# Kernel tuning notes

Measured on AMD Instinct MI355X. Metric: run time of the kernel, lower is better.

## Reference

```python
import jax, jax.numpy as jnp
import numpy as np

TAU = 0.2  # temperature from __init__
EPS = 1e-12  # F.normalize eps


def setup_inputs() -> dict:
    key = jax.random.key(0)
    k1, k2, k3 = jax.random.split(key, 3)
    N, D = 131072, 1024
    return {
        "query": jax.random.normal(k1, (D,), dtype=jnp.float32),
        "K": jax.random.normal(k2, (N, D), dtype=jnp.float32),
        "V": jax.random.normal(k3, (N, D), dtype=jnp.float32),
        "topk": 32,
    }


def reference(query, K, V, topk):
    # q = F.normalize(query, dim=-1)
    q = query / jnp.maximum(jnp.linalg.norm(query, axis=-1, keepdims=True), EPS)
    # logits: [N] cosine-sim / tau (K rows are assumed pre-normalized by write())
    logits = (K @ q) / TAU
    # top-k branch (N > topk)
    vals, idxs = jax.lax.top_k(logits, topk)          # [topk], [topk]
    attn = jax.nn.softmax(vals, axis=-1)              # [topk]
    out = attn @ V[idxs]                              # [D]
    full_attn = jnp.zeros_like(logits).at[idxs].set(attn)  # [N]
    return out, full_attn
```

## Files before the change

### kernel.cpp

```cpp
#include <hip/hip_runtime.h>
#include <float.h>
#include <math.h>

#define DIM    1024
#define NROWS  131072
#define TOPK   32
#define TAU    0.2f
#define CHUNK  512
#define NCHUNK (NROWS / CHUNK)
#define NCAND  (NCHUNK * TOPK)

#define LOG_BLOCKS 2048
#define ROWS_PER_WAVE 16
#define NITER 8

typedef float floatx4 __attribute__((ext_vector_type(4)));

__device__ __forceinline__ floatx4 ld_nt(const float* p) {
    return __builtin_nontemporal_load(reinterpret_cast<const floatx4*>(p));
}

__global__ __launch_bounds__(256) void logits_kernel(const float* __restrict__ Km,
                                                     const float* __restrict__ q,
                                                     float* __restrict__ logits,
                                                     float* __restrict__ full_attn) {
    const int t    = threadIdx.x;
    const int lane = t & 63;
    const int wave = t >> 6;
    const int sub  = lane & 31;
    const int rsel = lane >> 5;

    floatx4 qv[8];
    #pragma unroll
    for (int p = 0; p < 8; ++p)
        qv[p] = *reinterpret_cast<const floatx4*>(q + p * 128 + sub * 4);

    const int gwave = blockIdx.x * 4 + wave;
    const int rbase = gwave * ROWS_PER_WAVE;
    const float* kptr = Km + (size_t)(rbase + rsel) * DIM + sub * 4;

    floatx4 buf[2][8];
    #pragma unroll
    for (int p = 0; p < 8; ++p)
        buf[0][p] = ld_nt(kptr + p * 128);

    #pragma unroll
    for (int r = 0; r < NITER; ++r) {
        const float* knext = kptr + 2 * DIM;
        if (r < NITER - 1) {
            #pragma unroll
            for (int p = 0; p < 8; ++p)
                buf[(r + 1) & 1][p] = ld_nt(knext + p * 128);
        }
        float a0 = 0.f, a1 = 0.f, a2 = 0.f, a3 = 0.f;
        #pragma unroll
        for (int p = 0; p < 8; ++p) {
            floatx4 kv = buf[r & 1][p];
            floatx4 qq = qv[p];
            a0 = fmaf(kv.x, qq.x, a0);
            a1 = fmaf(kv.y, qq.y, a1);
            a2 = fmaf(kv.z, qq.z, a2);
            a3 = fmaf(kv.w, qq.w, a3);
        }
        float acc = (a0 + a1) + (a2 + a3);
        #pragma unroll
        for (int off = 1; off < 32; off <<= 1) acc += __shfl_xor(acc, off, 64);
        if (sub == 0) {
            const int row = rbase + 2 * r + rsel;
            logits[row]    = acc;
            full_attn[row] = 0.f;
        }
        kptr = knext;
    }
}

__global__ __launch_bounds__(64) void topk_local_kernel(const float* __restrict__ logits,
                                                        float* __restrict__ cand_val,
                                                        int* __restrict__ cand_idx) {
    const int lane = threadIdx.x;
    const int base = blockIdx.x * CHUNK;

    float v[8]; int gi[8];
    floatx4 a = *reinterpret_cast<const floatx4*>(logits + base + lane * 4);
    floatx4 b = *reinterpret_cast<const floatx4*>(logits + base + 256 + lane * 4);
    v[0] = a.x; v[1] = a.y; v[2] = a.z; v[3] = a.w;
    v[4] = b.x; v[5] = b.y; v[6] = b.z; v[7] = b.w;
    #pragma unroll
    for (int j = 0; j < 4; ++j) gi[j] = base + lane * 4 + j;
    #pragma unroll
    for (int j = 0; j < 4; ++j) gi[4 + j] = base + 256 + lane * 4 + j;

    for (int r = 0; r < TOPK; ++r) {
        float m = v[0]; int mi = gi[0];
        #pragma unroll
        for (int j = 1; j < 8; ++j)
            if (v[j] > m || (v[j] == m && gi[j] < mi)) { m = v[j]; mi = gi[j]; }
        #pragma unroll
        for (int off = 32; off > 0; off >>= 1) {
            float ov = __shfl_xor(m, off, 64);
            int   oi = __shfl_xor(mi, off, 64);
            if (ov > m || (ov == m && oi < mi)) { m = ov; mi = oi; }
        }
        #pragma unroll
        for (int j = 0; j < 8; ++j)
            if (gi[j] == mi) v[j] = -FLT_MAX;
        if (lane == 0) {
            cand_val[blockIdx.x * TOPK + r] = m;
            cand_idx[blockIdx.x * TOPK + r] = mi;
        }
    }
}

__global__ __launch_bounds__(256) void final_kernel(const float* __restrict__ cand_val,
                                                    const int* __restrict__ cand_idx,
                                                    const float* __restrict__ q,
                                                    const float* __restrict__ Vm,
                                                    float* __restrict__ out,
                                                    float* __restrict__ full_attn) {
    const int t = threadIdx.x;
    const int lane = t & 63, wave = t >> 6;
    __shared__ float wred_v[4];
    __shared__ int   wred_i[4];
    __shared__ float tval[TOPK];
    __shared__ int   tidx[TOPK];
    __shared__ float attn_s[TOPK];
    __shared__ float red4[4];
    __shared__ float scale_s;

    float ss = 0.f;
    for (int i = t; i < DIM; i += 256) { float vq = q[i]; ss = fmaf(vq, vq, ss); }
    #pragma unroll
    for (int off = 32; off > 0; off >>= 1) ss += __shfl_xor(ss, off, 64);
    if (lane == 0) red4[wave] = ss;
    __syncthreads();
    if (t == 0) {
        float s = red4[0] + red4[1] + red4[2] + red4[3];
        scale_s = 1.0f / (fmaxf(sqrtf(s), 1e-12f) * TAU);
    }

    float v[32]; int gi[32];
    #pragma unroll
    for (int k = 0; k < 32; ++k) {
        int c = t + 256 * k;
        v[k]  = cand_val[c];
        gi[k] = cand_idx[c];
    }
    float m = v[0]; int mi = gi[0];
    #pragma unroll
    for (int k = 1; k < 32; ++k)
        if (v[k] > m || (v[k] == m && gi[k] < mi)) { m = v[k]; mi = gi[k]; }

    __syncthreads();

    for (int r = 0; r < TOPK; ++r) {
        float wm = m; int wmi = mi;
        #pragma unroll
        for (int off = 32; off > 0; off >>= 1) {
            float ov = __shfl_xor(wm, off, 64);
            int   oi = __shfl_xor(wmi, off, 64);
            if (ov > wm || (ov == wm && oi < wmi)) { wm = ov; wmi = oi; }
        }
        if (lane == 0) { wred_v[wave] = wm; wred_i[wave] = wmi; }
        __syncthreads();
        float gm = wred_v[0]; int gmi = wred_i[0];
        #pragma unroll
        for (int w = 1; w < 4; ++w) {
            float ov = wred_v[w]; int oi = wred_i[w];
            if (ov > gm || (ov == gm && oi < gmi)) { gm = ov; gmi = oi; }
        }
        if (t == 0) { tval[r] = gm; tidx[r] = gmi; }
        if (mi == gmi) {
            #pragma unroll
            for (int k = 0; k < 32; ++k)
                if (gi[k] == gmi) v[k] = -FLT_MAX;
            m = v[0]; mi = gi[0];
            #pragma unroll
            for (int k = 1; k < 32; ++k)
                if (v[k] > m || (v[k] == m && gi[k] < mi)) { m = v[k]; mi = gi[k]; }
        }
        __syncthreads();
    }

    const float scale = scale_s;
    float sum = 0.f;
    #pragma unroll
    for (int j = 0; j < TOPK; ++j) sum += expf((tval[j] - tval[0]) * scale);
    if (t < TOPK) attn_s[t] = expf((tval[t] - tval[0]) * scale) / sum;
    __syncthreads();

    if (t < TOPK) full_attn[tidx[t]] = attn_s[t];

    for (int d = t; d < DIM; d += 256) {
        float acc = 0.f;
        #pragma unroll
        for (int j = 0; j < TOPK; ++j)
            acc = fmaf(attn_s[j], Vm[(size_t)tidx[j] * DIM + d], acc);
        out[d] = acc;
    }
}

extern "C" void kernel_launch(void* const* d_in, const int* in_sizes, int n_in,
                              void* d_out, int out_size, void* d_ws, size_t ws_size,
                              hipStream_t stream) {
    const float* q  = (const float*)d_in[0];
    const float* Km = (const float*)d_in[1];
    const float* Vm = (const float*)d_in[2];

    float* out       = (float*)d_out;
    float* full_attn = out + DIM;

    float* logits   = (float*)d_ws;
    float* cand_val = logits + NROWS;
    int*   cand_idx = (int*)(cand_val + NCAND);

    logits_kernel<<<LOG_BLOCKS, 256, 0, stream>>>(Km, q, logits, full_attn);
    topk_local_kernel<<<NCHUNK, 64, 0, stream>>>(logits, cand_val, cand_idx);
    final_kernel<<<1, 256, 0, stream>>>(cand_val, cand_idx, q, Vm, out, full_attn);
}
```

Measured before the change: 187.8 us.

## Split logits GEMV into per-lane partial sums plus separate reduction kernel

```diff
diff --git a/kernel.cpp b/kernel.cpp
--- a/kernel.cpp
+++ b/kernel.cpp
@@ -10,9 +10,8 @@
 #define NCHUNK (NROWS / CHUNK)
 #define NCAND  (NCHUNK * TOPK)
 
-#define LOG_BLOCKS 2048
-#define ROWS_PER_WAVE 16
-#define NITER 8
+#define NWAVES 8192
+#define WSTEPS 16
 
 typedef float floatx4 __attribute__((ext_vector_type(4)));
 
@@ -20,57 +19,70 @@
     return __builtin_nontemporal_load(reinterpret_cast<const floatx4*>(p));
 }
 
-__global__ __launch_bounds__(256) void logits_kernel(const float* __restrict__ Km,
-                                                     const float* __restrict__ q,
-                                                     float* __restrict__ logits,
-                                                     float* __restrict__ full_attn) {
+__global__ __launch_bounds__(256) void logitsA_kernel(const float* __restrict__ Km,
+                                                      const float* __restrict__ q,
+                                                      float* __restrict__ partial) {
     const int t    = threadIdx.x;
     const int lane = t & 63;
     const int wave = t >> 6;
-    const int sub  = lane & 31;
-    const int rsel = lane >> 5;
-
-    floatx4 qv[8];
-    #pragma unroll
-    for (int p = 0; p < 8; ++p)
-        qv[p] = *reinterpret_cast<const floatx4*>(q + p * 128 + sub * 4);
-
     const int gwave = blockIdx.x * 4 + wave;
-    const int rbase = gwave * ROWS_PER_WAVE;
-    const float* kptr = Km + (size_t)(rbase + rsel) * DIM + sub * 4;
-
-    floatx4 buf[2][8];
-    #pragma unroll
-    for (int p = 0; p < 8; ++p)
-        buf[0][p] = ld_nt(kptr + p * 128);
-
-    #pragma unroll
-    for (int r = 0; r < NITER; ++r) {
-        const float* knext = kptr + 2 * DIM;
-        if (r < NITER - 1) {
+
+    floatx4 qv[4];
+    #pragma unroll
+    for (int j = 0; j < 4; ++j)
+        qv[j] = *reinterpret_cast<const floatx4*>(q + j * 256 + lane * 4);
+
+    const float* base = Km + (size_t)gwave * DIM + lane * 4;
+    floatx4 b[2][4];
+    #pragma unroll
+    for (int j = 0; j < 4; ++j) b[0][j] = ld_nt(base + j * 256);
+
+    float part[WSTEPS];
+    #pragma unroll
+    for (int w = 0; w < WSTEPS; ++w) {
+        const float* nbase = base + (size_t)NWAVES * DIM;
+        if (w < WSTEPS - 1) {
             #pragma unroll
-            for (int p = 0; p < 8; ++p)
-                buf[(r + 1) & 1][p] = ld_nt(knext + p * 128);
+            for (int j = 0; j < 4; ++j) b[(w + 1) & 1][j] = ld_nt(nbase + j * 256);
         }
         float a0 = 0.f, a1 = 0.f, a2 = 0.f, a3 = 0.f;
         #pragma unroll
-        for (int p = 0; p < 8; ++p) {
-            floatx4 kv = buf[r & 1][p];
-            floatx4 qq = qv[p];
+        for (int j = 0; j < 4; ++j) {
+            floatx4 kv = b[w & 1][j];
+            floatx4 qq = qv[j];
             a0 = fmaf(kv.x, qq.x, a0);
             a1 = fmaf(kv.y, qq.y, a1);
             a2 = fmaf(kv.z, qq.z, a2);
             a3 = fmaf(kv.w, qq.w, a3);
         }
-        float acc = (a0 + a1) + (a2 + a3);
-        #pragma unroll
-        for (int off = 1; off < 32; off <<= 1) acc += __shfl_xor(acc, off, 64);
-        if (sub == 0) {
-            const int row = rbase + 2 * r + rsel;
-            logits[row]    = acc;
+        part[w] = (a0 + a1) + (a2 + a3);
+        base = nbase;
+    }
+    #pragma unroll
+    for (int w = 0; w < WSTEPS; ++w)
+        partial[(size_t)(gwave + NWAVES * w) * 64 + lane] = part[w];
+}
+
+__global__ __launch_bounds__(256) void reduceB_kernel(const float* __restrict__ partial,
+                                                      float* __restrict__ logits,
+                                                      float* __restrict__ full_attn) {
+    const int t    = threadIdx.x;
+    const int lane = t & 63;
+    const int wave = t >> 6;
+    const int gw   = blockIdx.x * 4 + wave;
+    const int rowbase = gw * 32;
+
+    #pragma unroll
+    for (int it = 0; it < 8; ++it) {
+        const int row = rowbase + it * 4 + (lane >> 4);
+        floatx4 v = *reinterpret_cast<const floatx4*>(partial + (size_t)row * 64 + (lane & 15) * 4);
+        float s = (v.x + v.y) + (v.z + v.w);
+        #pragma unroll
+        for (int off = 1; off < 16; off <<= 1) s += __shfl_xor(s, off, 64);
+        if ((lane & 15) == 0) {
+            logits[row]    = s;
             full_attn[row] = 0.f;
         }
-        kptr = knext;
     }
 }
 
@@ -212,8 +224,10 @@
     float* logits   = (float*)d_ws;
     float* cand_val = logits + NROWS;
     int*   cand_idx = (int*)(cand_val + NCAND);
-
-    logits_kernel<<<LOG_BLOCKS, 256, 0, stream>>>(Km, q, logits, full_attn);
+    float* partial  = (float*)(cand_idx + NCAND);
+
+    logitsA_kernel<<<NWAVES / 4, 256, 0, stream>>>(Km, q, partial);
+    reduceB_kernel<<<1024, 256, 0, stream>>>(partial, logits, full_attn);
     topk_local_kernel<<<NCHUNK, 64, 0, stream>>>(logits, cand_val, cand_idx);
     final_kernel<<<1, 256, 0, stream>>>(cand_val, cand_idx, q, Vm, out, full_attn);
 }
```

Result: slower. 210.9 us (+12.3%).

## Fuse logits computation with per-chunk local top-k in one kernel

Applied to the files above, without the earlier changes.

```diff
diff --git a/kernel.cpp b/kernel.cpp
--- a/kernel.cpp
+++ b/kernel.cpp
@@ -10,20 +10,19 @@
 #define NCHUNK (NROWS / CHUNK)
 #define NCAND  (NCHUNK * TOPK)
 
-#define LOG_BLOCKS 2048
-#define ROWS_PER_WAVE 16
-#define NITER 8
-
 typedef float floatx4 __attribute__((ext_vector_type(4)));
 
 __device__ __forceinline__ floatx4 ld_nt(const float* p) {
     return __builtin_nontemporal_load(reinterpret_cast<const floatx4*>(p));
 }
 
-__global__ __launch_bounds__(256) void logits_kernel(const float* __restrict__ Km,
-                                                     const float* __restrict__ q,
-                                                     float* __restrict__ logits,
-                                                     float* __restrict__ full_attn) {
+__global__ __launch_bounds__(512) void logits_topk_kernel(const float* __restrict__ Km,
+                                                          const float* __restrict__ q,
+                                                          float* __restrict__ cand_val,
+                                                          int* __restrict__ cand_idx,
+                                                          float* __restrict__ full_attn) {
+    __shared__ float loc[CHUNK];
+
     const int t    = threadIdx.x;
     const int lane = t & 63;
     const int wave = t >> 6;
@@ -35,8 +34,8 @@
     for (int p = 0; p < 8; ++p)
         qv[p] = *reinterpret_cast<const floatx4*>(q + p * 128 + sub * 4);
 
-    const int gwave = blockIdx.x * 4 + wave;
-    const int rbase = gwave * ROWS_PER_WAVE;
+    const int chunk_base = blockIdx.x * CHUNK;
+    const int rbase = chunk_base + wave * 64;
     const float* kptr = Km + (size_t)(rbase + rsel) * DIM + sub * 4;
 
     floatx4 buf[2][8];
@@ -45,9 +44,9 @@
         buf[0][p] = ld_nt(kptr + p * 128);
 
     #pragma unroll
-    for (int r = 0; r < NITER; ++r) {
+    for (int r = 0; r < 32; ++r) {
         const float* knext = kptr + 2 * DIM;
-        if (r < NITER - 1) {
+        if (r < 31) {
             #pragma unroll
             for (int p = 0; p < 8; ++p)
                 buf[(r + 1) & 1][p] = ld_nt(knext + p * 128);
@@ -67,46 +66,39 @@
         for (int off = 1; off < 32; off <<= 1) acc += __shfl_xor(acc, off, 64);
         if (sub == 0) {
             const int row = rbase + 2 * r + rsel;
-            logits[row]    = acc;
+            loc[row - chunk_base] = acc;
             full_attn[row] = 0.f;
         }
         kptr = knext;
     }
-}
-
-__global__ __launch_bounds__(64) void topk_local_kernel(const float* __restrict__ logits,
-                                                        float* __restrict__ cand_val,
-                                                        int* __restrict__ cand_idx) {
-    const int lane = threadIdx.x;
-    const int base = blockIdx.x * CHUNK;
-
-    float v[8]; int gi[8];
-    floatx4 a = *reinterpret_cast<const floatx4*>(logits + base + lane * 4);
-    floatx4 b = *reinterpret_cast<const floatx4*>(logits + base + 256 + lane * 4);
-    v[0] = a.x; v[1] = a.y; v[2] = a.z; v[3] = a.w;
-    v[4] = b.x; v[5] = b.y; v[6] = b.z; v[7] = b.w;
-    #pragma unroll
-    for (int j = 0; j < 4; ++j) gi[j] = base + lane * 4 + j;
-    #pragma unroll
-    for (int j = 0; j < 4; ++j) gi[4 + j] = base + 256 + lane * 4 + j;
-
-    for (int r = 0; r < TOPK; ++r) {
-        float m = v[0]; int mi = gi[0];
-        #pragma unroll
-        for (int j = 1; j < 8; ++j)
-            if (v[j] > m || (v[j] == m && gi[j] < mi)) { m = v[j]; mi = gi[j]; }
-        #pragma unroll
-        for (int off = 32; off > 0; off >>= 1) {
-            float ov = __shfl_xor(m, off, 64);
-            int   oi = __shfl_xor(mi, off, 64);
-            if (ov > m || (ov == m && oi < mi)) { m = ov; mi = oi; }
-        }
-        #pragma unroll
-        for (int j = 0; j < 8; ++j)
-            if (gi[j] == mi) v[j] = -FLT_MAX;
-        if (lane == 0) {
-            cand_val[blockIdx.x * TOPK + r] = m;
-            cand_idx[blockIdx.x * TOPK + r] = mi;
+
+    __syncthreads();
+
+    if (wave == 0) {
+        float v[8]; int gi[8];
+        #pragma unroll
+        for (int j = 0; j < 8; ++j) {
+            v[j]  = loc[lane * 8 + j];
+            gi[j] = chunk_base + lane * 8 + j;
+        }
+        for (int r = 0; r < TOPK; ++r) {
+            float m = v[0]; int mi = gi[0];
+            #pragma unroll
+            for (int j = 1; j < 8; ++j)
+                if (v[j] > m || (v[j] == m && gi[j] < mi)) { m = v[j]; mi = gi[j]; }
+            #pragma unroll
+            for (int off = 32; off > 0; off >>= 1) {
+                float ov = __shfl_xor(m, off, 64);
+                int   oi = __shfl_xor(mi, off, 64);
+                if (ov > m || (ov == m && oi < mi)) { m = ov; mi = oi; }
+            }
+            #pragma unroll
+            for (int j = 0; j < 8; ++j)
+                if (gi[j] == mi) v[j] = -FLT_MAX;
+            if (lane == 0) {
+                cand_val[blockIdx.x * TOPK + r] = m;
+                cand_idx[blockIdx.x * TOPK + r] = mi;
+            }
         }
     }
 }
@@ -209,11 +201,9 @@
     float* out       = (float*)d_out;
     float* full_attn = out + DIM;
 
-    float* logits   = (float*)d_ws;
-    float* cand_val = logits + NROWS;
+    float* cand_val = (float*)d_ws;
     int*   cand_idx = (int*)(cand_val + NCAND);
 
-    logits_kernel<<<LOG_BLOCKS, 256, 0, stream>>>(Km, q, logits, full_attn);
-    topk_local_kernel<<<NCHUNK, 64, 0, stream>>>(logits, cand_val, cand_idx);
+    logits_topk_kernel<<<NCHUNK, 512, 0, stream>>>(Km, q, cand_val, cand_idx, full_attn);
     final_kernel<<<1, 256, 0, stream>>>(cand_val, cand_idx, q, Vm, out, full_attn);
 }
```

Result: no change. 185.1 us (-1.4%).
